# Performance work log

Measured on AMD Instinct MI355X. Metric: run time of the kernel, lower is better.

The kernel has to match this reference:

```python
import jax, jax.numpy as jnp
import numpy as np

N = 100000      # nodes
E = 1600000     # edges per adjacency
NFEAT = 128
NHID = 128


def _digcn_conv(x, w, b, src, dst, edge_attr, num_nodes):
    # x @ W, then gather source, scale by edge weight, scatter-add to dst (PyG add-aggr)
    h = x @ w                                   # [N, out]
    msg = edge_attr[:, None] * h[src]           # [E, out]
    out = jax.ops.segment_sum(msg, dst, num_segments=num_nodes)
    return out + b


def _inception(x, ln_w, ln_b, c1_w, c1_b, c2_w, c2_b,
               edge_index, edge_attr, edge_index2, edge_attr2):
    x0 = x @ ln_w + ln_b
    x1 = _digcn_conv(x, c1_w, c1_b, edge_index[0], edge_index[1], edge_attr, x.shape[0])
    x2 = _digcn_conv(x, c2_w, c2_b, edge_index2[0], edge_index2[1], edge_attr2, x.shape[0])
    # eval mode: dropout is identity; the module sums the three branches
    return x0 + x1 + x2


def _mk_params(key, dims):
    ps = {}
    blocks = [("b1", NFEAT, NHID), ("b2", NHID, NHID), ("b3", NHID, NHID)]
    for name, din, dout in blocks:
        for pfx in ("ln", "c1", "c2"):
            key, k1 = jax.random.split(key)
            ps[f"{name}_{pfx}_w"] = jax.random.normal(k1, (din, dout), jnp.float32) * (1.0 / np.sqrt(din))
            ps[f"{name}_{pfx}_b"] = jnp.zeros((dout,), jnp.float32)
    return ps


def setup_inputs() -> dict:
    key = jax.random.key(0)
    ks = jax.random.split(key, 8)
    inp = {
        "x": jax.random.normal(ks[0], (N, NFEAT), jnp.float32),
        "edge_index": jax.random.randint(ks[1], (2, E), 0, N, jnp.int64 if jax.config.jax_enable_x64 else jnp.int32).astype(jnp.int32),
        "edge_attr": jax.random.uniform(ks[2], (E,), jnp.float32),
        "edge_index2": jax.random.randint(ks[3], (2, E), 0, N).astype(jnp.int32),
        "edge_attr2": jax.random.uniform(ks[4], (E,), jnp.float32),
    }
    inp.update(_mk_params(ks[5], None))
    return inp


def reference(x, edge_index, edge_attr, edge_index2, edge_attr2,
              b1_ln_w, b1_ln_b, b1_c1_w, b1_c1_b, b1_c2_w, b1_c2_b,
              b2_ln_w, b2_ln_b, b2_c1_w, b2_c1_b, b2_c2_w, b2_c2_b,
              b3_ln_w, b3_ln_b, b3_c1_w, b3_c1_b, b3_c2_w, b3_c2_b):
    x = _inception(x, b1_ln_w, b1_ln_b, b1_c1_w, b1_c1_b, b1_c2_w, b1_c2_b,
                   edge_index, edge_attr, edge_index2, edge_attr2)
    x = _inception(x, b2_ln_w, b2_ln_b, b2_c1_w, b2_c1_b, b2_c2_w, b2_c2_b,
                   edge_index, edge_attr, edge_index2, edge_attr2)
    x = _inception(x, b3_ln_w, b3_ln_b, b3_c1_w, b3_c1_b, b3_c2_w, b3_c2_b,
                   edge_index, edge_attr, edge_index2, edge_attr2)
    # torch module splits x per-graph via data.batch (data-dependent shapes);
    # we return the full node embedding matrix [N, NHID] instead.
    return x
```

## Files before the change

### kernel.cpp

```cpp
#include <hip/hip_runtime.h>

#define DIM 128
#define CHUNK 8192
#define NBK 256
#define BSHIFT 10

typedef __attribute__((ext_vector_type(8))) short bf16x8;
typedef __attribute__((ext_vector_type(4))) float f32x4;
typedef __attribute__((ext_vector_type(2))) unsigned u32x2;
typedef __attribute__((ext_vector_type(4))) unsigned u32x4;

static __device__ __forceinline__ short f2bf(float f) {
    union { float f; unsigned u; } v; v.f = f;
    unsigned r = (v.u + 0x7FFF + ((v.u >> 16) & 1)) >> 16;
    return (short)r;
}
static __device__ __forceinline__ float asf(unsigned u) {
    union { unsigned u; float f; } v; v.u = u; return v.f;
}
static __device__ __forceinline__ unsigned asu(float f) {
    union { float f; unsigned u; } v; v.f = f; return v.u;
}
static __device__ __forceinline__ unsigned pk2(float a, float b) {
    return (unsigned)(unsigned short)f2bf(a) | ((unsigned)(unsigned short)f2bf(b) << 16);
}

struct WPtrs { const float* w[9]; };
__global__ __launch_bounds__(256) void prep_w_k(WPtrs p, short* __restrict__ wt)
{
    const int g = blockIdx.x * 256 + threadIdx.x;
    if (g >= 3 * 12 * 8 * 64) return;
    const int lane = g & 63;
    const int ct   = (g >> 6) & 7;
    const int rest = g >> 9;
    const int ks   = rest % 12;
    const int layer = rest / 12;
    const int mat   = ks >> 2;
    const int n     = ct * 16 + (lane & 15);
    const int kbase = (ks & 3) * 32 + (lane >> 4) * 8;
    const float* W = p.w[layer * 3 + mat];
    short* dst = wt + (size_t)layer * 49152 + ks * 4096 + ct * 512 + lane * 8;
#pragma unroll
    for (int j = 0; j < 8; ++j) dst[j] = f2bf(W[(size_t)(kbase + j) * DIM + n]);
}

__global__ __launch_bounds__(256) void cast_k(
    const float* __restrict__ X, short* __restrict__ Xb, int n8)
{
    const int i = blockIdx.x * 256 + threadIdx.x;
    if (i >= n8) return;
    const float4* xp = (const float4*)X + (size_t)i * 2;
    const float4 a = xp[0];
    const float4 b = xp[1];
    bf16x8 v;
    v[0] = f2bf(a.x); v[1] = f2bf(a.y); v[2] = f2bf(a.z); v[3] = f2bf(a.w);
    v[4] = f2bf(b.x); v[5] = f2bf(b.y); v[6] = f2bf(b.z); v[7] = f2bf(b.w);
    *(bf16x8*)(Xb + (size_t)i * 8) = v;
}


__global__ __launch_bounds__(256) void p0_bhist_k(
    const int* __restrict__ d1, const int* __restrict__ d2,
    int* __restrict__ bcnt, int N, int E, int E2)
{
    __shared__ int lh[NBK];
    const int t = threadIdx.x;
    lh[t] = 0;
    __syncthreads();
    const int stride = gridDim.x * 256;
    for (int i = blockIdx.x * 256 + t; i < E;  i += stride) atomicAdd(&lh[d1[i] >> BSHIFT], 1);
    for (int i = blockIdx.x * 256 + t; i < E2; i += stride) atomicAdd(&lh[(N + d2[i]) >> BSHIFT], 1);
    __syncthreads();
    if (lh[t]) atomicAdd(&bcnt[t], lh[t]);
}

__global__ __launch_bounds__(256) void bscan_k(
    const int* __restrict__ bcnt, int* __restrict__ bktbase,
    int* __restrict__ cursor, int* __restrict__ rowptr, int twoN, int ET)
{
    __shared__ int sv[NBK];
    const int t = threadIdx.x;
    sv[t] = bcnt[t];
    __syncthreads();
    for (int off = 1; off < NBK; off <<= 1) {
        int a = (t >= off) ? sv[t - off] : 0;
        __syncthreads();
        sv[t] += a;
        __syncthreads();
    }
    const int excl = t ? sv[t - 1] : 0;
    bktbase[t] = excl;
    cursor[t]  = excl;
    if (t == 0) rowptr[twoN] = ET;
}

__global__ __launch_bounds__(256) void p1_bin_k(
    const int* __restrict__ s1, const int* __restrict__ d1, const float* __restrict__ ea1,
    const int* __restrict__ s2, const int* __restrict__ d2, const float* __restrict__ ea2,
    int* __restrict__ cursor, uint2* __restrict__ binned,
    int N, int E, int E2, int nc1)
{
    __shared__ __align__(16) uint2 stage[CHUNK];
    __shared__ unsigned char lbkt[CHUNK];
    __shared__ int hist[NBK], exclv[NBK], lcur[NBK], gpos[NBK];

    const int t = threadIdx.x;
    const int c = blockIdx.x;
    const bool a2 = (c >= nc1);
    const int* S  = a2 ? s2  : s1;
    const int* D  = a2 ? d2  : d1;
    const float* W = a2 ? ea2 : ea1;
    const int Eloc = a2 ? E2 : E;
    const int voff = a2 ? N : 0;
    const int eb   = (a2 ? (c - nc1) : c) * CHUNK;
    const int ec   = min(CHUNK, Eloc - eb);

    hist[t] = 0;
    __syncthreads();

    for (int i = t; i < ec; i += 256)
        atomicAdd(&hist[(unsigned)(voff + D[eb + i]) >> BSHIFT], 1);
    __syncthreads();

    exclv[t] = hist[t];
    __syncthreads();
    for (int off = 1; off < NBK; off <<= 1) {
        int a = (t >= off) ? exclv[t - off] : 0;
        __syncthreads();
        exclv[t] += a;
        __syncthreads();
    }
    const int myincl = exclv[t];
    __syncthreads();
    exclv[t] = myincl - hist[t];
    lcur[t]  = exclv[t];
    if (hist[t]) gpos[t] = atomicAdd(&cursor[t], hist[t]);
    __syncthreads();

    for (int i = t; i < ec; i += 256) {
        const int v = voff + D[eb + i];
        const int b = (unsigned)v >> BSHIFT;
        const int lpos = atomicAdd(&lcur[b], 1);
        stage[lpos] = make_uint2((unsigned)S[eb + i] | ((unsigned)(v & 1023) << 17),
                                 asu(W[eb + i]));
        lbkt[lpos] = (unsigned char)b;
    }
    __syncthreads();

    for (int s = t; s < ec; s += 256) {
        const int b = lbkt[s];
        binned[gpos[b] + (s - exclv[b])] = stage[s];
    }
}

__global__ __launch_bounds__(256) void p2_final_k(
    const uint2* __restrict__ binned, const int* __restrict__ bktbase,
    int* __restrict__ rowptr, uint2* __restrict__ pairs, int twoN)
{
    __shared__ int hist[1024], scn[1024], lcur[1024];
    const int t = threadIdx.x;
    const int b = blockIdx.x;
    const int base = bktbase[b];
    const int cnt  = bktbase[b + 1] - base;
    const int vbase = b << BSHIFT;

    for (int i = t; i < 1024; i += 256) hist[i] = 0;
    __syncthreads();

    for (int i = t; i < cnt; i += 256)
        atomicAdd(&hist[binned[base + i].x >> 17], 1);
    __syncthreads();

    for (int i = t; i < 1024; i += 256) scn[i] = hist[i];
    __syncthreads();
    for (int off = 1; off < 1024; off <<= 1) {
        int a0 = (t       >= off) ? scn[t       - off] : 0;
        int a1 = (t + 256 >= off) ? scn[t + 256 - off] : 0;
        int a2 = (t + 512 >= off) ? scn[t + 512 - off] : 0;
        int a3 = (t + 768 >= off) ? scn[t + 768 - off] : 0;
        __syncthreads();
        scn[t] += a0; scn[t + 256] += a1; scn[t + 512] += a2; scn[t + 768] += a3;
        __syncthreads();
    }
    for (int i = t; i < 1024; i += 256) {
        const int excl = scn[i] - hist[i];
        lcur[i] = excl;
        const int v = vbase + i;
        if (v < twoN) rowptr[v] = base + excl;
    }
    __syncthreads();

    for (int i = t; i < cnt; i += 256) {
        const uint2 e = binned[base + i];
        const int vlow = e.x >> 17;
        const int pos = base + atomicAdd(&lcur[vlow], 1);
        pairs[pos] = make_uint2(e.x & 0x1FFFFu, e.y);
    }
}

static __device__ __forceinline__ void bf2acc8(unsigned w, u32x4 h, float* acc)
{
    const float wf = asf(w);
    acc[0] = fmaf(wf, asf(h.x << 16),         acc[0]);
    acc[1] = fmaf(wf, asf(h.x & 0xFFFF0000u), acc[1]);
    acc[2] = fmaf(wf, asf(h.y << 16),         acc[2]);
    acc[3] = fmaf(wf, asf(h.y & 0xFFFF0000u), acc[3]);
    acc[4] = fmaf(wf, asf(h.z << 16),         acc[4]);
    acc[5] = fmaf(wf, asf(h.z & 0xFFFF0000u), acc[5]);
    acc[6] = fmaf(wf, asf(h.w << 16),         acc[6]);
    acc[7] = fmaf(wf, asf(h.w & 0xFFFF0000u), acc[7]);
}

static __device__ __forceinline__ void gacc16(
    const short* __restrict__ H, const uint2* __restrict__ pairs,
    int start, int end, int s, float* acc)
{
    int j = start;
    for (; j + 7 < end; j += 8) {
        u32x2 p[8]; u32x4 h[8];
#pragma unroll
        for (int q = 0; q < 8; ++q)
            p[q] = __builtin_nontemporal_load((const u32x2*)(pairs + j + q));
#pragma unroll
        for (int q = 0; q < 8; ++q)
            h[q] = *(const u32x4*)(H + (size_t)p[q].x * DIM + s * 8);
#pragma unroll
        for (int q = 0; q < 8; ++q) bf2acc8(p[q].y, h[q], acc);
    }
    if (j + 3 < end) {
        u32x2 p[4]; u32x4 h[4];
#pragma unroll
        for (int q = 0; q < 4; ++q)
            p[q] = __builtin_nontemporal_load((const u32x2*)(pairs + j + q));
#pragma unroll
        for (int q = 0; q < 4; ++q)
            h[q] = *(const u32x4*)(H + (size_t)p[q].x * DIM + s * 8);
#pragma unroll
        for (int q = 0; q < 4; ++q) bf2acc8(p[q].y, h[q], acc);
        j += 4;
    }
    for (; j < end; ++j) {
        const u32x2 p = __builtin_nontemporal_load((const u32x2*)(pairs + j));
        const u32x4 h = *(const u32x4*)(H + (size_t)p.x * DIM + s * 8);
        bf2acc8(p.y, h, acc);
    }
}

__global__ __launch_bounds__(256, 4) void fused_layer_k(
    const short* __restrict__ Xb, const short* __restrict__ Wp,
    const uint2* __restrict__ pairs, const int* __restrict__ rowptr,
    const float* __restrict__ b0, const float* __restrict__ b1,
    const float* __restrict__ b2,
    float* __restrict__ Yf, short* __restrict__ Yb, int N)
{
    __shared__ __align__(16) short As[64][272];
    const int t  = threadIdx.x;
    const int m0 = blockIdx.x * 64;

    const int s    = t & 15;
    const int nrow = t >> 4;
#pragma unroll
    for (int nl = 0; nl < 4; ++nl) {
        const int r    = nl * 16 + nrow;
        const int node = m0 + r;
        float a1[8] = {0.f,0.f,0.f,0.f,0.f,0.f,0.f,0.f};
        float a2[8] = {0.f,0.f,0.f,0.f,0.f,0.f,0.f,0.f};
        if (node < N) {
            gacc16(Xb, pairs, rowptr[node],     rowptr[node + 1],     s, a1);
            gacc16(Xb, pairs, rowptr[N + node], rowptr[N + node + 1], s, a2);
        }
        u32x4 o1 = (u32x4){pk2(a1[0], a1[1]), pk2(a1[2], a1[3]),
                           pk2(a1[4], a1[5]), pk2(a1[6], a1[7])};
        u32x4 o2 = (u32x4){pk2(a2[0], a2[1]), pk2(a2[2], a2[3]),
                           pk2(a2[4], a2[5]), pk2(a2[6], a2[7])};
        *(u32x4*)&As[r][s * 8]       = o1;
        *(u32x4*)&As[r][128 + s * 8] = o2;
    }
    __syncthreads();

    const int wave  = t >> 6;
    const int lane  = t & 63;
    const int l15   = lane & 15;
    const int kq    = lane >> 4;
    const int mbase = wave * 16;
    const int mrow  = m0 + mbase + l15;
    const int mclmp = (mrow < N) ? mrow : (N - 1);
    const short* xrow = Xb + (size_t)mclmp * DIM + kq * 8;

    f32x4 acc[8];
#pragma unroll
    for (int ct = 0; ct < 8; ++ct) acc[ct] = (f32x4){0.f, 0.f, 0.f, 0.f};

#pragma unroll
    for (int ks = 0; ks < 4; ++ks) {
        const bf16x8 a = *(const bf16x8*)(xrow + ks * 32);
        const short* wb = Wp + ks * 4096 + lane * 8;
#pragma unroll
        for (int ct = 0; ct < 8; ++ct)
            acc[ct] = __builtin_amdgcn_mfma_f32_16x16x32_bf16(
                a, *(const bf16x8*)(wb + ct * 512), acc[ct], 0, 0, 0);
    }
#pragma unroll
    for (int ks = 4; ks < 12; ++ks) {
        const bf16x8 a = *(const bf16x8*)&As[mbase + l15][(ks - 4) * 32 + kq * 8];
        const short* wb = Wp + ks * 4096 + lane * 8;
#pragma unroll
        for (int ct = 0; ct < 8; ++ct)
            acc[ct] = __builtin_amdgcn_mfma_f32_16x16x32_bf16(
                a, *(const bf16x8*)(wb + ct * 512), acc[ct], 0, 0, 0);
    }

#pragma unroll
    for (int ct = 0; ct < 8; ++ct) {
        const int col = ct * 16 + l15;
        const float bias = b0[col] + b1[col] + b2[col];
#pragma unroll
        for (int r = 0; r < 4; ++r) {
            const int m = m0 + mbase + kq * 4 + r;
            if (m >= N) continue;
            const float v = acc[ct][r] + bias;
            if (Yf) __builtin_nontemporal_store(v, &Yf[(size_t)m * DIM + col]);
            else    Yb[(size_t)m * DIM + col] = f2bf(v);
        }
    }
}

extern "C" void kernel_launch(void* const* d_in, const int* in_sizes, int n_in,
                              void* d_out, int out_size, void* d_ws, size_t ws_size,
                              hipStream_t stream)
{
    const float* x   = (const float*)d_in[0];
    const int*   ei  = (const int*)d_in[1];
    const float* ea  = (const float*)d_in[2];
    const int*   ei2 = (const int*)d_in[3];
    const float* ea2 = (const float*)d_in[4];

    const int N  = in_sizes[0] / DIM;
    const int E  = in_sizes[2];
    const int E2 = in_sizes[4];
    const int ET = E + E2;

    float* OUT = (float*)d_out;

    short* Xb0 = (short*)d_ws;
    short* Xb1 = Xb0 + (size_t)N * DIM;
    short* WT  = Xb1 + (size_t)N * DIM;
    int*   rowptr = (int*)(WT + 3 * 49152);
    int*   bcnt   = rowptr + 2 * N + 4;
    int*   bktbase= bcnt + NBK;
    int*   cursor = bktbase + NBK + 4;
    uint2* pairs  = (uint2*)(cursor + NBK);
    uint2* binned = pairs + ET;

    WPtrs wp;
    for (int b = 0; b < 3; ++b) {
        wp.w[b * 3 + 0] = (const float*)d_in[5 + 6 * b + 0];
        wp.w[b * 3 + 1] = (const float*)d_in[5 + 6 * b + 2];
        wp.w[b * 3 + 2] = (const float*)d_in[5 + 6 * b + 4];
    }
    prep_w_k<<<(18432 + 255) / 256, 256, 0, stream>>>(wp, WT);

    const int n8 = N * DIM / 8;
    cast_k<<<(n8 + 255) / 256, 256, 0, stream>>>(x, Xb0, n8);

    const int nc1 = (E + CHUNK - 1) / CHUNK;
    const int nc2 = (E2 + CHUNK - 1) / CHUNK;
    const int nbk_used = (2 * N + (1 << BSHIFT) - 1) >> BSHIFT;

    hipMemsetAsync(bcnt, 0, NBK * sizeof(int), stream);
    p0_bhist_k<<<256, 256, 0, stream>>>(ei + E, ei2 + E2, bcnt, N, E, E2);
    bscan_k<<<1, NBK, 0, stream>>>(bcnt, bktbase, cursor, rowptr, 2 * N, ET);
    p1_bin_k<<<nc1 + nc2, 256, 0, stream>>>(ei, ei + E, ea, ei2, ei2 + E2, ea2,
                                            cursor, binned, N, E, E2, nc1);
    p2_final_k<<<nbk_used, 256, 0, stream>>>(binned, bktbase, rowptr, pairs, 2 * N);

    const int gGemm = (N + 63) / 64;

    const short* cur = Xb0;
    for (int b = 0; b < 3; ++b) {
        const float* lnb = (const float*)d_in[5 + 6 * b + 1];
        const float* c1b = (const float*)d_in[5 + 6 * b + 3];
        const float* c2b = (const float*)d_in[5 + 6 * b + 5];

        float* yf = (b == 2) ? OUT : nullptr;
        short* yb = (b == 2) ? nullptr : ((cur == Xb0) ? Xb1 : Xb0);

        fused_layer_k<<<gGemm, 256, 0, stream>>>(
            cur, WT + (size_t)b * 49152, pairs, rowptr, lnb, c1b, c2b, yf, yb, N);

        if (b < 2) cur = yb;
    }
}
```

Baseline: 785.1 us.

## Replace two-pass bucketed CSR build with atomic histogram, scan and scatter

Drops the bucket-then-sort CSR construction and instead counts per-node in-degree with global atomics, runs a three-kernel prefix scan, and scatters edges with per-node atomic cursors. It also swaps the LDS padding in the fused layer for an XOR swizzle and raises the occupancy hint to 5 blocks per CU. The scatter writes are random and non-deterministic in order within a row, which costs more DRAM traffic than the staged binned writes and may change floating-point summation order. Removing the padding shrinks shared memory to allow the higher occupancy.

```diff
diff --git a/kernel.cpp b/kernel.cpp
--- a/kernel.cpp
+++ b/kernel.cpp
@@ -1,9 +1,8 @@
 #include <hip/hip_runtime.h>
 
 #define DIM 128
-#define CHUNK 8192
-#define NBK 256
-#define BSHIFT 10
+#define SCAN_T 256
+#define SCAN_E 16
 
 typedef __attribute__((ext_vector_type(8))) short bf16x8;
 typedef __attribute__((ext_vector_type(4))) float f32x4;
@@ -59,142 +58,92 @@
 }
 
 
-__global__ __launch_bounds__(256) void p0_bhist_k(
+__global__ __launch_bounds__(256) void hist_k(
     const int* __restrict__ d1, const int* __restrict__ d2,
-    int* __restrict__ bcnt, int N, int E, int E2)
-{
-    __shared__ int lh[NBK];
+    int* __restrict__ cnt, int N, int E, int E2)
+{
+    const int stride = gridDim.x * 256;
+    for (int i = blockIdx.x * 256 + threadIdx.x; i < E;  i += stride)
+        atomicAdd(&cnt[d1[i]], 1);
+    for (int i = blockIdx.x * 256 + threadIdx.x; i < E2; i += stride)
+        atomicAdd(&cnt[N + d2[i]], 1);
+}
+
+__global__ __launch_bounds__(256) void scan1_k(
+    const int* __restrict__ cnt, int* __restrict__ partial, int total)
+{
+    __shared__ int sd[SCAN_T];
     const int t = threadIdx.x;
-    lh[t] = 0;
+    const int base = blockIdx.x * SCAN_T * SCAN_E + t * SCAN_E;
+    int s = 0;
+#pragma unroll
+    for (int j = 0; j < SCAN_E; ++j) {
+        const int idx = base + j;
+        if (idx < total) s += cnt[idx];
+    }
+    sd[t] = s;
     __syncthreads();
-    const int stride = gridDim.x * 256;
-    for (int i = blockIdx.x * 256 + t; i < E;  i += stride) atomicAdd(&lh[d1[i] >> BSHIFT], 1);
-    for (int i = blockIdx.x * 256 + t; i < E2; i += stride) atomicAdd(&lh[(N + d2[i]) >> BSHIFT], 1);
+    for (int off = 128; off > 0; off >>= 1) {
+        if (t < off) sd[t] += sd[t + off];
+        __syncthreads();
+    }
+    if (t == 0) partial[blockIdx.x] = sd[0];
+}
+
+__global__ void scan2_k(int* __restrict__ partial, int nblk,
+                        int* __restrict__ rowptr, int twoN, int ET)
+{
+    if (threadIdx.x == 0 && blockIdx.x == 0) {
+        int run = 0;
+        for (int i = 0; i < nblk; ++i) { const int v = partial[i]; partial[i] = run; run += v; }
+        rowptr[twoN] = ET;
+    }
+}
+
+__global__ __launch_bounds__(256) void scan3_k(
+    const int* __restrict__ cnt, const int* __restrict__ partial,
+    int* __restrict__ rowptr, int* __restrict__ cursor, int total)
+{
+    __shared__ int sd[SCAN_T];
+    const int t = threadIdx.x;
+    const int base = blockIdx.x * SCAN_T * SCAN_E + t * SCAN_E;
+    int loc[SCAN_E];
+    int s = 0;
+#pragma unroll
+    for (int j = 0; j < SCAN_E; ++j) {
+        const int idx = base + j;
+        const int v = (idx < total) ? cnt[idx] : 0;
+        loc[j] = v; s += v;
+    }
+    sd[t] = s;
     __syncthreads();
-    if (lh[t]) atomicAdd(&bcnt[t], lh[t]);
-}
-
-__global__ __launch_bounds__(256) void bscan_k(
-    const int* __restrict__ bcnt, int* __restrict__ bktbase,
-    int* __restrict__ cursor, int* __restrict__ rowptr, int twoN, int ET)
-{
-    __shared__ int sv[NBK];
-    const int t = threadIdx.x;
-    sv[t] = bcnt[t];
-    __syncthreads();
-    for (int off = 1; off < NBK; off <<= 1) {
-        int a = (t >= off) ? sv[t - off] : 0;
+    for (int off = 1; off < SCAN_T; off <<= 1) {
+        const int a = (t >= off) ? sd[t - off] : 0;
         __syncthreads();
-        sv[t] += a;
+        sd[t] += a;
         __syncthreads();
     }
-    const int excl = t ? sv[t - 1] : 0;
-    bktbase[t] = excl;
-    cursor[t]  = excl;
-    if (t == 0) rowptr[twoN] = ET;
-}
-
-__global__ __launch_bounds__(256) void p1_bin_k(
+    int excl = sd[t] - s + partial[blockIdx.x];
+#pragma unroll
+    for (int j = 0; j < SCAN_E; ++j) {
+        const int idx = base + j;
+        if (idx < total) { rowptr[idx] = excl; cursor[idx] = excl; excl += loc[j]; }
+    }
+}
+
+__global__ __launch_bounds__(256) void scat_k(
     const int* __restrict__ s1, const int* __restrict__ d1, const float* __restrict__ ea1,
     const int* __restrict__ s2, const int* __restrict__ d2, const float* __restrict__ ea2,
-    int* __restrict__ cursor, uint2* __restrict__ binned,
-    int N, int E, int E2, int nc1)
-{
-    __shared__ __align__(16) uint2 stage[CHUNK];
-    __shared__ unsigned char lbkt[CHUNK];
-    __shared__ int hist[NBK], exclv[NBK], lcur[NBK], gpos[NBK];
-
-    const int t = threadIdx.x;
-    const int c = blockIdx.x;
-    const bool a2 = (c >= nc1);
-    const int* S  = a2 ? s2  : s1;
-    const int* D  = a2 ? d2  : d1;
-    const float* W = a2 ? ea2 : ea1;
-    const int Eloc = a2 ? E2 : E;
-    const int voff = a2 ? N : 0;
-    const int eb   = (a2 ? (c - nc1) : c) * CHUNK;
-    const int ec   = min(CHUNK, Eloc - eb);
-
-    hist[t] = 0;
-    __syncthreads();
-
-    for (int i = t; i < ec; i += 256)
-        atomicAdd(&hist[(unsigned)(voff + D[eb + i]) >> BSHIFT], 1);
-    __syncthreads();
-
-    exclv[t] = hist[t];
-    __syncthreads();
-    for (int off = 1; off < NBK; off <<= 1) {
-        int a = (t >= off) ? exclv[t - off] : 0;
-        __syncthreads();
-        exclv[t] += a;
-        __syncthreads();
-    }
-    const int myincl = exclv[t];
-    __syncthreads();
-    exclv[t] = myincl - hist[t];
-    lcur[t]  = exclv[t];
-    if (hist[t]) gpos[t] = atomicAdd(&cursor[t], hist[t]);
-    __syncthreads();
-
-    for (int i = t; i < ec; i += 256) {
-        const int v = voff + D[eb + i];
-        const int b = (unsigned)v >> BSHIFT;
-        const int lpos = atomicAdd(&lcur[b], 1);
-        stage[lpos] = make_uint2((unsigned)S[eb + i] | ((unsigned)(v & 1023) << 17),
-                                 asu(W[eb + i]));
-        lbkt[lpos] = (unsigned char)b;
-    }
-    __syncthreads();
-
-    for (int s = t; s < ec; s += 256) {
-        const int b = lbkt[s];
-        binned[gpos[b] + (s - exclv[b])] = stage[s];
-    }
-}
-
-__global__ __launch_bounds__(256) void p2_final_k(
-    const uint2* __restrict__ binned, const int* __restrict__ bktbase,
-    int* __restrict__ rowptr, uint2* __restrict__ pairs, int twoN)
-{
-    __shared__ int hist[1024], scn[1024], lcur[1024];
-    const int t = threadIdx.x;
-    const int b = blockIdx.x;
-    const int base = bktbase[b];
-    const int cnt  = bktbase[b + 1] - base;
-    const int vbase = b << BSHIFT;
-
-    for (int i = t; i < 1024; i += 256) hist[i] = 0;
-    __syncthreads();
-
-    for (int i = t; i < cnt; i += 256)
-        atomicAdd(&hist[binned[base + i].x >> 17], 1);
-    __syncthreads();
-
-    for (int i = t; i < 1024; i += 256) scn[i] = hist[i];
-    __syncthreads();
-    for (int off = 1; off < 1024; off <<= 1) {
-        int a0 = (t       >= off) ? scn[t       - off] : 0;
-        int a1 = (t + 256 >= off) ? scn[t + 256 - off] : 0;
-        int a2 = (t + 512 >= off) ? scn[t + 512 - off] : 0;
-        int a3 = (t + 768 >= off) ? scn[t + 768 - off] : 0;
-        __syncthreads();
-        scn[t] += a0; scn[t + 256] += a1; scn[t + 512] += a2; scn[t + 768] += a3;
-        __syncthreads();
-    }
-    for (int i = t; i < 1024; i += 256) {
-        const int excl = scn[i] - hist[i];
-        lcur[i] = excl;
-        const int v = vbase + i;
-        if (v < twoN) rowptr[v] = base + excl;
-    }
-    __syncthreads();
-
-    for (int i = t; i < cnt; i += 256) {
-        const uint2 e = binned[base + i];
-        const int vlow = e.x >> 17;
-        const int pos = base + atomicAdd(&lcur[vlow], 1);
-        pairs[pos] = make_uint2(e.x & 0x1FFFFu, e.y);
+    int* __restrict__ cursor, uint2* __restrict__ pairs, int N, int E, int E2)
+{
+    const int stride = gridDim.x * 256;
+    for (int i = blockIdx.x * 256 + threadIdx.x; i < E; i += stride) {
+        const int pos = atomicAdd(&cursor[d1[i]], 1);
+        pairs[pos] = make_uint2((unsigned)s1[i], asu(ea1[i]));
+    }
+    for (int i = blockIdx.x * 256 + threadIdx.x; i < E2; i += stride) {
+        const int pos = atomicAdd(&cursor[N + d2[i]], 1);
+        pairs[pos] = make_uint2((unsigned)s2[i], asu(ea2[i]));
     }
 }
 
@@ -246,14 +195,14 @@
     }
 }
 
-__global__ __launch_bounds__(256, 4) void fused_layer_k(
+__global__ __launch_bounds__(256, 5) void fused_layer_k(
     const short* __restrict__ Xb, const short* __restrict__ Wp,
     const uint2* __restrict__ pairs, const int* __restrict__ rowptr,
     const float* __restrict__ b0, const float* __restrict__ b1,
     const float* __restrict__ b2,
     float* __restrict__ Yf, short* __restrict__ Yb, int N)
 {
-    __shared__ __align__(16) short As[64][272];
+    __shared__ __align__(16) short As[64][256];
     const int t  = threadIdx.x;
     const int m0 = blockIdx.x * 64;
 
@@ -273,8 +222,9 @@
                            pk2(a1[4], a1[5]), pk2(a1[6], a1[7])};
         u32x4 o2 = (u32x4){pk2(a2[0], a2[1]), pk2(a2[2], a2[3]),
                            pk2(a2[4], a2[5]), pk2(a2[6], a2[7])};
-        *(u32x4*)&As[r][s * 8]       = o1;
-        *(u32x4*)&As[r][128 + s * 8] = o2;
+        const int sw = s ^ (r & 7);
+        *(u32x4*)&As[r][sw * 8]        = o1;
+        *(u32x4*)&As[r][128 + sw * 8]  = o2;
     }
     __syncthreads();
 
@@ -302,7 +252,10 @@
     }
 #pragma unroll
     for (int ks = 4; ks < 12; ++ks) {
-        const bf16x8 a = *(const bf16x8*)&As[mbase + l15][(ks - 4) * 32 + kq * 8];
+        const int lin  = (ks - 4) * 4 + kq;
+        const int row  = mbase + l15;
+        const int slot = (lin & 16) | ((lin & 15) ^ (row & 7));
+        const bf16x8 a = *(const bf16x8*)&As[row][slot * 8];
         const short* wb = Wp + ks * 4096 + lane * 8;
 #pragma unroll
         for (int ct = 0; ct < 8; ++ct)
@@ -339,6 +292,7 @@
     const int E  = in_sizes[2];
     const int E2 = in_sizes[4];
     const int ET = E + E2;
+    const int twoN = 2 * N;
 
     float* OUT = (float*)d_out;
 
@@ -346,11 +300,10 @@
     short* Xb1 = Xb0 + (size_t)N * DIM;
     short* WT  = Xb1 + (size_t)N * DIM;
     int*   rowptr = (int*)(WT + 3 * 49152);
-    int*   bcnt   = rowptr + 2 * N + 4;
-    int*   bktbase= bcnt + NBK;
-    int*   cursor = bktbase + NBK + 4;
-    uint2* pairs  = (uint2*)(cursor + NBK);
-    uint2* binned = pairs + ET;
+    int*   cnt    = rowptr + twoN + 4;
+    int*   cursor = cnt + twoN;
+    int*   partial= cursor + twoN;
+    uint2* pairs  = (uint2*)(partial + 256);
 
     WPtrs wp;
     for (int b = 0; b < 3; ++b) {
@@ -363,16 +316,14 @@
     const int n8 = N * DIM / 8;
     cast_k<<<(n8 + 255) / 256, 256, 0, stream>>>(x, Xb0, n8);
 
-    const int nc1 = (E + CHUNK - 1) / CHUNK;
-    const int nc2 = (E2 + CHUNK - 1) / CHUNK;
-    const int nbk_used = (2 * N + (1 << BSHIFT) - 1) >> BSHIFT;
-
-    hipMemsetAsync(bcnt, 0, NBK * sizeof(int), stream);
-    p0_bhist_k<<<256, 256, 0, stream>>>(ei + E, ei2 + E2, bcnt, N, E, E2);
-    bscan_k<<<1, NBK, 0, stream>>>(bcnt, bktbase, cursor, rowptr, 2 * N, ET);
-    p1_bin_k<<<nc1 + nc2, 256, 0, stream>>>(ei, ei + E, ea, ei2, ei2 + E2, ea2,
-                                            cursor, binned, N, E, E2, nc1);
-    p2_final_k<<<nbk_used, 256, 0, stream>>>(binned, bktbase, rowptr, pairs, 2 * N);
+    const int nscan = (twoN + SCAN_T * SCAN_E - 1) / (SCAN_T * SCAN_E);
+    hipMemsetAsync(cnt, 0, (size_t)twoN * sizeof(int), stream);
+    hist_k<<<1024, 256, 0, stream>>>(ei + E, ei2 + E2, cnt, N, E, E2);
+    scan1_k<<<nscan, 256, 0, stream>>>(cnt, partial, twoN);
+    scan2_k<<<1, 64, 0, stream>>>(partial, nscan, rowptr, twoN, ET);
+    scan3_k<<<nscan, 256, 0, stream>>>(cnt, partial, rowptr, cursor, twoN);
+    scat_k<<<1024, 256, 0, stream>>>(ei, ei + E, ea, ei2, ei2 + E2, ea2,
+                                     cursor, pairs, N, E, E2);
 
     const int gGemm = (N + 63) / 64;
 
```

Result: slower. 1.051 ms (+33.9%).

## Split fused layer into two aggregate-then-MFMA phases with halved shared tile

Applied to the files above, without the earlier changes.

The kernel now aggregates the first adjacency, runs its MFMA slice, then reuses the same shared-memory tile for the second adjacency's aggregation and MFMA slice. This halves the LDS tile (64x144 instead of 64x272) and the launch-bound occupancy hint rises from 4 to 8 blocks per SM. The aim is more resident waves to hide the latency of the gather-heavy aggregation. The cost is an extra barrier and serialized phases within each block, and the register budget per thread is tighter under the higher occupancy target, which could cause spills with 8 f32x4 accumulators live.

```diff
diff --git a/kernel.cpp b/kernel.cpp
--- a/kernel.cpp
+++ b/kernel.cpp
@@ -246,37 +246,19 @@
     }
 }
 
-__global__ __launch_bounds__(256, 4) void fused_layer_k(
+__global__ __launch_bounds__(256, 8) void fused_layer_k(
     const short* __restrict__ Xb, const short* __restrict__ Wp,
     const uint2* __restrict__ pairs, const int* __restrict__ rowptr,
     const float* __restrict__ b0, const float* __restrict__ b1,
     const float* __restrict__ b2,
     float* __restrict__ Yf, short* __restrict__ Yb, int N)
 {
-    __shared__ __align__(16) short As[64][272];
+    __shared__ __align__(16) short As[64][144];
     const int t  = threadIdx.x;
     const int m0 = blockIdx.x * 64;
 
     const int s    = t & 15;
     const int nrow = t >> 4;
-#pragma unroll
-    for (int nl = 0; nl < 4; ++nl) {
-        const int r    = nl * 16 + nrow;
-        const int node = m0 + r;
-        float a1[8] = {0.f,0.f,0.f,0.f,0.f,0.f,0.f,0.f};
-        float a2[8] = {0.f,0.f,0.f,0.f,0.f,0.f,0.f,0.f};
-        if (node < N) {
-            gacc16(Xb, pairs, rowptr[node],     rowptr[node + 1],     s, a1);
-            gacc16(Xb, pairs, rowptr[N + node], rowptr[N + node + 1], s, a2);
-        }
-        u32x4 o1 = (u32x4){pk2(a1[0], a1[1]), pk2(a1[2], a1[3]),
-                           pk2(a1[4], a1[5]), pk2(a1[6], a1[7])};
-        u32x4 o2 = (u32x4){pk2(a2[0], a2[1]), pk2(a2[2], a2[3]),
-                           pk2(a2[4], a2[5]), pk2(a2[6], a2[7])};
-        *(u32x4*)&As[r][s * 8]       = o1;
-        *(u32x4*)&As[r][128 + s * 8] = o2;
-    }
-    __syncthreads();
 
     const int wave  = t >> 6;
     const int lane  = t & 63;
@@ -292,6 +274,19 @@
     for (int ct = 0; ct < 8; ++ct) acc[ct] = (f32x4){0.f, 0.f, 0.f, 0.f};
 
 #pragma unroll
+    for (int nl = 0; nl < 4; ++nl) {
+        const int r    = nl * 16 + nrow;
+        const int node = m0 + r;
+        float a[8] = {0.f,0.f,0.f,0.f,0.f,0.f,0.f,0.f};
+        if (node < N)
+            gacc16(Xb, pairs, rowptr[node], rowptr[node + 1], s, a);
+        u32x4 o = (u32x4){pk2(a[0], a[1]), pk2(a[2], a[3]),
+                          pk2(a[4], a[5]), pk2(a[6], a[7])};
+        *(u32x4*)&As[r][s * 8] = o;
+    }
+    __syncthreads();
+
+#pragma unroll
     for (int ks = 0; ks < 4; ++ks) {
         const bf16x8 a = *(const bf16x8*)(xrow + ks * 32);
         const short* wb = Wp + ks * 4096 + lane * 8;
@@ -301,8 +296,32 @@
                 a, *(const bf16x8*)(wb + ct * 512), acc[ct], 0, 0, 0);
     }
 #pragma unroll
-    for (int ks = 4; ks < 12; ++ks) {
+    for (int ks = 4; ks < 8; ++ks) {
         const bf16x8 a = *(const bf16x8*)&As[mbase + l15][(ks - 4) * 32 + kq * 8];
+        const short* wb = Wp + ks * 4096 + lane * 8;
+#pragma unroll
+        for (int ct = 0; ct < 8; ++ct)
+            acc[ct] = __builtin_amdgcn_mfma_f32_16x16x32_bf16(
+                a, *(const bf16x8*)(wb + ct * 512), acc[ct], 0, 0, 0);
+    }
+    __syncthreads();
+
+#pragma unroll
+    for (int nl = 0; nl < 4; ++nl) {
+        const int r    = nl * 16 + nrow;
+        const int node = m0 + r;
+        float a[8] = {0.f,0.f,0.f,0.f,0.f,0.f,0.f,0.f};
+        if (node < N)
+            gacc16(Xb, pairs, rowptr[N + node], rowptr[N + node + 1], s, a);
+        u32x4 o = (u32x4){pk2(a[0], a[1]), pk2(a[2], a[3]),
+                          pk2(a[4], a[5]), pk2(a[6], a[7])};
+        *(u32x4*)&As[r][s * 8] = o;
+    }
+    __syncthreads();
+
+#pragma unroll
+    for (int ks = 8; ks < 12; ++ks) {
+        const bf16x8 a = *(const bf16x8*)&As[mbase + l15][(ks - 8) * 32 + kq * 8];
         const short* wb = Wp + ks * 4096 + lane * 8;
 #pragma unroll
         for (int ct = 0; ct < 8; ++ct)
```

Result: slower. 826.4 us (+5.3%).
